# Performance work log

Measured on AMD Instinct MI355X. Metric: run time of the kernel, lower is better.

The kernel has to match this reference:

```python
import jax, jax.numpy as jnp
import numpy as np

RES = 128          # occupancy grid resolution per axis
S = 320            # fixed number of marching steps per ray
STEP = 0.01        # render_step_size
NEAR = 0.0         # near_plane
ALPHA_THRE = 0.01  # alpha_sample_thre


def setup_inputs() -> dict:
    key = jax.random.key(0)
    k1, k2, k3 = jax.random.split(key, 3)
    N = 16384
    # ray origins inside the scene aabb [-1,1]^3
    origins = (jax.random.uniform(k1, (N, 3), dtype=jnp.float32) - 0.5)
    d = jax.random.normal(k2, (N, 3), dtype=jnp.float32)
    directions = d / jnp.linalg.norm(d, axis=-1, keepdims=True)
    # per-cell densities of the occupancy grid (occupancy_grid.occs)
    occs = jax.random.uniform(k3, (RES, RES, RES), dtype=jnp.float32)
    aabb = jnp.array([[-1.0, -1.0, -1.0], [1.0, 1.0, 1.0]], dtype=jnp.float32)
    return {"origins": origins, "directions": directions, "occs": occs, "aabb": aabb}


def _ray_aabb(o, d, aabb):
    # robust slab intersection; returns (t_min, t_max) per ray
    safe_d = jnp.where(jnp.abs(d) < 1e-10, 1e-10, d)
    inv = 1.0 / safe_d
    t0 = (aabb[0] - o) * inv
    t1 = (aabb[1] - o) * inv
    tmin = jnp.max(jnp.minimum(t0, t1), axis=-1)
    tmax = jnp.min(jnp.maximum(t0, t1), axis=-1)
    return jnp.maximum(tmin, NEAR), tmax


def reference(origins, directions, occs, aabb):
    N = origins.shape[0]
    tmin, tmax = _ray_aabb(origins, directions, aabb)           # [N]
    i = jnp.arange(S, dtype=origins.dtype)
    t_starts = tmin[:, None] + i[None, :] * STEP                # [N,S]
    t_ends = t_starts + STEP
    t_mid = 0.5 * (t_starts + t_ends)
    # sample midpoints along each ray: [N,S,3]
    pos = origins[:, None, :] + directions[:, None, :] * t_mid[..., None]
    # occupancy-grid query (nerfacc.grid._query style)
    u = (pos - aabb[0]) / (aabb[1] - aabb[0])                   # [N,S,3] in [0,1)
    idx = jnp.clip(jnp.floor(u * RES).astype(jnp.int32), 0, RES - 1)
    occ = occs[idx[..., 0], idx[..., 1], idx[..., 2]]           # [N,S] gather
    inside = jnp.all((u >= 0.0) & (u < 1.0), axis=-1)           # [N,S]
    # alpha = 1 - exp(-render_step_size * density), as in update_binary_grid
    alpha = 1.0 - jnp.exp(-occ * STEP)
    mask = inside & (t_ends <= tmax[:, None]) & (alpha > ALPHA_THRE) \
           & (tmax[:, None] > tmin[:, None])                    # [N,S]
    ray_indices = jnp.broadcast_to(
        jnp.arange(N, dtype=jnp.int32)[:, None], mask.shape)
    maskf = mask.astype(pos.dtype)
    positions = pos * maskf[..., None]                          # compacted-by-mask
    return (positions,
            t_starts * maskf,
            t_ends * maskf,
            jnp.where(mask, ray_indices, -1),
            mask)
```

## Files before the change

### kernel.cpp

```cpp
#include <hip/hip_runtime.h>

#define RES 128
#define NSTEPS 320
#define STEP 0.01f
#define OCC_THRE 1.0050336f

#define SPT 4
#define TPR (NSTEPS / SPT)
#define BLOCK 256

__global__ __launch_bounds__(BLOCK) void nerfacc_sampler_kernel(
    const float* __restrict__ origins,
    const float* __restrict__ dirs,
    const float* __restrict__ occs,
    const float* __restrict__ aabb,
    float* __restrict__ out,
    int N)
{
    const int T = blockIdx.x * BLOCK + threadIdx.x;
    const int r = T / TPR;
    if (r >= N) return;
    const int j0 = (T - r * TPR) * SPT;

    const float ox = origins[r * 3 + 0];
    const float oy = origins[r * 3 + 1];
    const float oz = origins[r * 3 + 2];
    const float dx = dirs[r * 3 + 0];
    const float dy = dirs[r * 3 + 1];
    const float dz = dirs[r * 3 + 2];
    const float lx = aabb[0], ly = aabb[1], lz = aabb[2];
    const float hx = aabb[3], hy = aabb[4], hz = aabb[5];

    const float sdx = (fabsf(dx) < 1e-10f) ? 1e-10f : dx;
    const float sdy = (fabsf(dy) < 1e-10f) ? 1e-10f : dy;
    const float sdz = (fabsf(dz) < 1e-10f) ? 1e-10f : dz;
    const float ivx = 1.0f / sdx, ivy = 1.0f / sdy, ivz = 1.0f / sdz;
    const float t0x = (lx - ox) * ivx, t1x = (hx - ox) * ivx;
    const float t0y = (ly - oy) * ivy, t1y = (hy - oy) * ivy;
    const float t0z = (lz - oz) * ivz, t1z = (hz - oz) * ivz;
    float tmin = fmaxf(fmaxf(fminf(t0x, t1x), fminf(t0y, t1y)), fminf(t0z, t1z));
    float tmax = fminf(fminf(fmaxf(t0x, t1x), fmaxf(t0y, t1y)), fmaxf(t0z, t1z));
    tmin = fmaxf(tmin, 0.0f);

    float px[SPT], py[SPT], pz[SPT], ts[SPT], te[SPT], ri[SPT], mm[SPT];
    float occv[SPT];

    int gidx[SPT];
    float uxv[SPT], uyv[SPT], uzv[SPT];
    #pragma unroll
    for (int i = 0; i < SPT; ++i) {
        const float t_start = tmin + (float)(j0 + i) * STEP;
        const float t_end   = t_start + STEP;
        const float t_mid   = 0.5f * (t_start + t_end);
        const float x = ox + dx * t_mid;
        const float y = oy + dy * t_mid;
        const float z = oz + dz * t_mid;
        const float ux = (x - lx) / (hx - lx);
        const float uy = (y - ly) / (hy - ly);
        const float uz = (z - lz) / (hz - lz);
        int ix = min(max((int)floorf(ux * (float)RES), 0), RES - 1);
        int iy = min(max((int)floorf(uy * (float)RES), 0), RES - 1);
        int iz = min(max((int)floorf(uz * (float)RES), 0), RES - 1);
        gidx[i] = (ix * RES + iy) * RES + iz;
        uxv[i] = ux; uyv[i] = uy; uzv[i] = uz;
        px[i] = x; py[i] = y; pz[i] = z;
        ts[i] = t_start; te[i] = t_end;
    }
    #pragma unroll
    for (int i = 0; i < SPT; ++i) occv[i] = occs[gidx[i]];

    #pragma unroll
    for (int i = 0; i < SPT; ++i) {
        const bool inside = (uxv[i] >= 0.0f) & (uxv[i] < 1.0f) &
                            (uyv[i] >= 0.0f) & (uyv[i] < 1.0f) &
                            (uzv[i] >= 0.0f) & (uzv[i] < 1.0f);
        const bool mask = inside & (te[i] <= tmax) & (occv[i] > OCC_THRE) & (tmax > tmin);
        const float m = mask ? 1.0f : 0.0f;
        px[i] *= m; py[i] *= m; pz[i] *= m;
        ts[i] *= m; te[i] *= m;
        ri[i] = mask ? (float)r : -1.0f;
        mm[i] = m;
    }

    const size_t NS   = (size_t)N * NSTEPS;
    const size_t base = (size_t)r * NSTEPS + (size_t)j0;

    float4* pp = (float4*)(out + base * 3);
    pp[0] = make_float4(px[0], py[0], pz[0], px[1]);
    pp[1] = make_float4(py[1], pz[1], px[2], py[2]);
    pp[2] = make_float4(pz[2], px[3], py[3], pz[3]);

    *(float4*)(out + NS * 3 + base) = make_float4(ts[0], ts[1], ts[2], ts[3]);
    *(float4*)(out + NS * 4 + base) = make_float4(te[0], te[1], te[2], te[3]);
    *(float4*)(out + NS * 5 + base) = make_float4(ri[0], ri[1], ri[2], ri[3]);
    *(float4*)(out + NS * 6 + base) = make_float4(mm[0], mm[1], mm[2], mm[3]);
}

extern "C" void kernel_launch(void* const* d_in, const int* in_sizes, int n_in,
                              void* d_out, int out_size, void* d_ws, size_t ws_size,
                              hipStream_t stream) {
    const float* origins = (const float*)d_in[0];
    const float* dirs    = (const float*)d_in[1];
    const float* occs    = (const float*)d_in[2];
    const float* aabb    = (const float*)d_in[3];
    float* out = (float*)d_out;

    const int N = in_sizes[0] / 3;
    const int total = N * TPR;
    const int grid = (total + BLOCK - 1) / BLOCK;

    nerfacc_sampler_kernel<<<dim3(grid), dim3(BLOCK), 0, stream>>>(
        origins, dirs, occs, aabb, out, N);
}
```

Baseline: 180.2 us.

## Pack occupancy grid into bitfield and use nontemporal output stores

A pre-pass kernel thresholds the 8 MB float occupancy grid into a 256 KB bitmask in workspace, and the sampler then gathers 32-bit words and tests single bits instead of gathering floats. This shrinks the gather working set so it stays in cache, at the cost of an extra kernel launch that reads the full grid once per call. The output writes also become nontemporal stores, which keeps the large streaming output from evicting cached data.

```diff
diff --git a/kernel.cpp b/kernel.cpp
--- a/kernel.cpp
+++ b/kernel.cpp
@@ -1,4 +1,5 @@
 #include <hip/hip_runtime.h>
+#include <stdint.h>
 
 #define RES 128
 #define NSTEPS 320
@@ -9,10 +10,32 @@
 #define TPR (NSTEPS / SPT)
 #define BLOCK 256
 
+#define NCELLS (RES * RES * RES)
+#define NWORDS (NCELLS / 32)
+
+typedef float v4f __attribute__((ext_vector_type(4)));
+
+__global__ __launch_bounds__(256) void build_bits_kernel(
+    const float* __restrict__ occs, uint32_t* __restrict__ bits)
+{
+    const int w = blockIdx.x * 256 + threadIdx.x;
+    const v4f* p = (const v4f*)(occs + (size_t)w * 32);
+    uint32_t m = 0;
+    #pragma unroll
+    for (int q = 0; q < 8; ++q) {
+        const v4f v = p[q];
+        m |= (v.x > OCC_THRE ? 1u : 0u) << (q * 4 + 0);
+        m |= (v.y > OCC_THRE ? 1u : 0u) << (q * 4 + 1);
+        m |= (v.z > OCC_THRE ? 1u : 0u) << (q * 4 + 2);
+        m |= (v.w > OCC_THRE ? 1u : 0u) << (q * 4 + 3);
+    }
+    bits[w] = m;
+}
+
 __global__ __launch_bounds__(BLOCK) void nerfacc_sampler_kernel(
     const float* __restrict__ origins,
     const float* __restrict__ dirs,
-    const float* __restrict__ occs,
+    const uint32_t* __restrict__ bits,
     const float* __restrict__ aabb,
     float* __restrict__ out,
     int N)
@@ -43,10 +66,10 @@
     tmin = fmaxf(tmin, 0.0f);
 
     float px[SPT], py[SPT], pz[SPT], ts[SPT], te[SPT], ri[SPT], mm[SPT];
-    float occv[SPT];
+    float uxv[SPT], uyv[SPT], uzv[SPT];
+    int bidx[SPT];
+    uint32_t wv[SPT];
 
-    int gidx[SPT];
-    float uxv[SPT], uyv[SPT], uzv[SPT];
     #pragma unroll
     for (int i = 0; i < SPT; ++i) {
         const float t_start = tmin + (float)(j0 + i) * STEP;
@@ -61,20 +84,21 @@
         int ix = min(max((int)floorf(ux * (float)RES), 0), RES - 1);
         int iy = min(max((int)floorf(uy * (float)RES), 0), RES - 1);
         int iz = min(max((int)floorf(uz * (float)RES), 0), RES - 1);
-        gidx[i] = (ix * RES + iy) * RES + iz;
+        bidx[i] = (ix * RES + iy) * RES + iz;
         uxv[i] = ux; uyv[i] = uy; uzv[i] = uz;
         px[i] = x; py[i] = y; pz[i] = z;
         ts[i] = t_start; te[i] = t_end;
     }
     #pragma unroll
-    for (int i = 0; i < SPT; ++i) occv[i] = occs[gidx[i]];
+    for (int i = 0; i < SPT; ++i) wv[i] = bits[bidx[i] >> 5];
 
     #pragma unroll
     for (int i = 0; i < SPT; ++i) {
         const bool inside = (uxv[i] >= 0.0f) & (uxv[i] < 1.0f) &
                             (uyv[i] >= 0.0f) & (uyv[i] < 1.0f) &
                             (uzv[i] >= 0.0f) & (uzv[i] < 1.0f);
-        const bool mask = inside & (te[i] <= tmax) & (occv[i] > OCC_THRE) & (tmax > tmin);
+        const bool occ_hit = (wv[i] >> (bidx[i] & 31)) & 1u;
+        const bool mask = inside & (te[i] <= tmax) & occ_hit & (tmax > tmin);
         const float m = mask ? 1.0f : 0.0f;
         px[i] *= m; py[i] *= m; pz[i] *= m;
         ts[i] *= m; te[i] *= m;
@@ -85,15 +109,19 @@
     const size_t NS   = (size_t)N * NSTEPS;
     const size_t base = (size_t)r * NSTEPS + (size_t)j0;
 
-    float4* pp = (float4*)(out + base * 3);
-    pp[0] = make_float4(px[0], py[0], pz[0], px[1]);
-    pp[1] = make_float4(py[1], pz[1], px[2], py[2]);
-    pp[2] = make_float4(pz[2], px[3], py[3], pz[3]);
+    v4f* pp = (v4f*)(out + base * 3);
+    __builtin_nontemporal_store((v4f){px[0], py[0], pz[0], px[1]}, pp + 0);
+    __builtin_nontemporal_store((v4f){py[1], pz[1], px[2], py[2]}, pp + 1);
+    __builtin_nontemporal_store((v4f){pz[2], px[3], py[3], pz[3]}, pp + 2);
 
-    *(float4*)(out + NS * 3 + base) = make_float4(ts[0], ts[1], ts[2], ts[3]);
-    *(float4*)(out + NS * 4 + base) = make_float4(te[0], te[1], te[2], te[3]);
-    *(float4*)(out + NS * 5 + base) = make_float4(ri[0], ri[1], ri[2], ri[3]);
-    *(float4*)(out + NS * 6 + base) = make_float4(mm[0], mm[1], mm[2], mm[3]);
+    __builtin_nontemporal_store((v4f){ts[0], ts[1], ts[2], ts[3]},
+                                (v4f*)(out + NS * 3 + base));
+    __builtin_nontemporal_store((v4f){te[0], te[1], te[2], te[3]},
+                                (v4f*)(out + NS * 4 + base));
+    __builtin_nontemporal_store((v4f){ri[0], ri[1], ri[2], ri[3]},
+                                (v4f*)(out + NS * 5 + base));
+    __builtin_nontemporal_store((v4f){mm[0], mm[1], mm[2], mm[3]},
+                                (v4f*)(out + NS * 6 + base));
 }
 
 extern "C" void kernel_launch(void* const* d_in, const int* in_sizes, int n_in,
@@ -104,11 +132,14 @@
     const float* occs    = (const float*)d_in[2];
     const float* aabb    = (const float*)d_in[3];
     float* out = (float*)d_out;
+    uint32_t* bits = (uint32_t*)d_ws;
 
     const int N = in_sizes[0] / 3;
+
+    build_bits_kernel<<<dim3(NWORDS / 256), dim3(256), 0, stream>>>(occs, bits);
+
     const int total = N * TPR;
     const int grid = (total + BLOCK - 1) / BLOCK;
-
     nerfacc_sampler_kernel<<<dim3(grid), dim3(BLOCK), 0, stream>>>(
-        origins, dirs, occs, aabb, out, N);
+        origins, dirs, bits, aabb, out, N);
 }
```

New measurement: 189.3 us. 5.0% more time.
